# Kernel tuning notes

Measured on AMD Instinct MI355X. Metric: run time of the kernel, lower is better.

The kernel has to match this reference:

```python
import jax, jax.numpy as jnp
import numpy as np

EMBED_DIM = 1024
NUM_HEADS = 16
HEAD_DIM = EMBED_DIM // NUM_HEADS
B, L = 32, 2049
LN_EPS = 1e-5


def setup_inputs() -> dict:
    key = jax.random.key(0)
    ks = jax.random.split(key, 11)
    s = 1.0 / np.sqrt(EMBED_DIM)
    x = jax.random.normal(ks[0], (B, L, EMBED_DIM), dtype=jnp.float32)
    Wq = jax.random.normal(ks[1], (EMBED_DIM, EMBED_DIM), dtype=jnp.float32) * s
    bq = jnp.zeros((EMBED_DIM,), dtype=jnp.float32)
    Wk = jax.random.normal(ks[2], (EMBED_DIM, EMBED_DIM), dtype=jnp.float32) * s
    bk = jnp.zeros((EMBED_DIM,), dtype=jnp.float32)
    Wv = jax.random.normal(ks[3], (EMBED_DIM, EMBED_DIM), dtype=jnp.float32) * s
    bv = jnp.zeros((EMBED_DIM,), dtype=jnp.float32)
    Wo = jax.random.normal(ks[4], (EMBED_DIM, EMBED_DIM), dtype=jnp.float32) * s
    bo = jnp.zeros((EMBED_DIM,), dtype=jnp.float32)
    ln_g = jnp.ones((EMBED_DIM,), dtype=jnp.float32)
    ln_b = jnp.zeros((EMBED_DIM,), dtype=jnp.float32)
    return {"x": x, "Wq": Wq, "bq": bq, "Wk": Wk, "bk": bk, "Wv": Wv,
            "bv": bv, "Wo": Wo, "bo": bo, "ln_g": ln_g, "ln_b": ln_b}


def reference(x, Wq, bq, Wk, bk, Wv, bv, Wo, bo, ln_g, ln_b):
    # x: [B, L, D]; CLS token attends to the other L-1 tokens (dropout = eval/identity)
    cls_tok = x[:, 0, :]              # [B, D]
    others = x[:, 1:, :]              # [B, L-1, D]
    q = cls_tok @ Wq.T + bq           # [B, D]
    k = others @ Wk.T + bk            # [B, L-1, D]
    v = others @ Wv.T + bv            # [B, L-1, D]
    q = q.reshape(q.shape[0], NUM_HEADS, HEAD_DIM)                       # [B, H, d]
    k = k.reshape(k.shape[0], k.shape[1], NUM_HEADS, HEAD_DIM)           # [B, S, H, d]
    v = v.reshape(v.shape[0], v.shape[1], NUM_HEADS, HEAD_DIM)           # [B, S, H, d]
    scores = jnp.einsum('bhd,bshd->bhs', q, k) / np.sqrt(HEAD_DIM)       # [B, H, S]
    w = jax.nn.softmax(scores, axis=-1)
    attn = jnp.einsum('bhs,bshd->bhd', w, v)                             # [B, H, d]
    attn = attn.reshape(attn.shape[0], NUM_HEADS * HEAD_DIM)             # [B, D]
    out = attn @ Wo.T + bo
    y = out + cls_tok
    mu = jnp.mean(y, axis=-1, keepdims=True)
    var = jnp.var(y, axis=-1, keepdims=True)
    return (y - mu) / jnp.sqrt(var + LN_EPS) * ln_g + ln_b               # [B, D]
```

## Files before the change

kernel.cpp:

```cpp
#include <hip/hip_runtime.h>
#include <math.h>

#define B_ 32
#define L_ 2049
#define E_ 1024
#define H_ 16
#define NT_ 8
#define STILE 256

#define OFF_Q     0
#define OFF_T     (OFF_Q + B_*E_)
#define OFF_QBK   (OFF_T + B_*H_*E_)
#define OFF_M     (OFF_QBK + B_*H_)
#define OFF_L     (OFF_M + B_*NT_*H_)
#define OFF_U     (OFF_L + B_*NT_*H_)
#define OFF_ATTN  (OFF_U + B_*H_*E_)
#define OFF_Y     (OFF_ATTN + B_*E_)
#define OFF_UP    (OFF_Y + B_*E_)

__global__ __launch_bounds__(256) void k_gemm32(const float* __restrict__ A, long long As, int mode,
                                                const float* __restrict__ W,
                                                const float* __restrict__ bias,
                                                const float* __restrict__ resid, long long Rs,
                                                float* __restrict__ C) {
    __shared__ float wls[2 * 1056];
    const int j0 = blockIdx.x * 2, tid = threadIdx.x;
    #pragma unroll
    for (int k = 0; k < 2; ++k) {
        int idx4 = k * 256 + tid;
        int row = idx4 >> 8, c4 = idx4 & 255;
        float4 v = *(const float4*)(W + (size_t)(j0 + row) * E_ + 4 * c4);
        *(float4*)&wls[row * 1056 + 4 * c4 + ((c4 >> 5) << 2)] = v;
    }
    __syncthreads();
    const int bb = tid >> 3, kseg = tid & 7;
    const long long kbase = (mode == 1) ? (long long)(j0 >> 6) * E_ : 0;
    const float* arow = A + (size_t)bb * As + kbase + kseg * 128;
    float a0 = 0.f, a1 = 0.f;
    #pragma unroll 4
    for (int i = 0; i < 32; ++i) {
        float4 av = *(const float4*)(arow + 4 * i);
        const float* wb = &wls[kseg * 132 + 4 * i];
        float4 w0 = *(const float4*)(wb);
        float4 w1 = *(const float4*)(wb + 1056);
        a0 += av.x * w0.x + av.y * w0.y + av.z * w0.z + av.w * w0.w;
        a1 += av.x * w1.x + av.y * w1.y + av.z * w1.z + av.w * w1.w;
    }
    #pragma unroll
    for (int off = 4; off; off >>= 1) {
        a0 += __shfl_down(a0, off, 8);
        a1 += __shfl_down(a1, off, 8);
    }
    if (kseg == 0) {
        float r0 = a0 + bias[j0], r1 = a1 + bias[j0 + 1];
        if (resid) {
            r0 += resid[(size_t)bb * Rs + j0];
            r1 += resid[(size_t)bb * Rs + j0 + 1];
        }
        C[(size_t)bb * E_ + j0] = r0;
        C[(size_t)bb * E_ + j0 + 1] = r1;
    }
}

__global__ __launch_bounds__(256) void k_tproj(const float* __restrict__ Wk,
                                               const float* __restrict__ bk,
                                               float* __restrict__ ws) {
    __shared__ float qs[64 * 33];
    __shared__ float wls[64 * 68];
    const int h = blockIdx.x, e0 = blockIdx.y * 64, tid = threadIdx.x;
    const float* q = ws + OFF_Q;
    #pragma unroll
    for (int k = 0; k < 8; ++k) {
        int idx = k * 256 + tid;
        int b = idx >> 6, d = idx & 63;
        qs[d * 33 + b] = q[(size_t)b * E_ + 64 * h + d];
    }
    #pragma unroll
    for (int k = 0; k < 4; ++k) {
        int idx4 = k * 256 + tid;
        int d = idx4 >> 4, c4 = idx4 & 15;
        float4 v = *(const float4*)(Wk + (size_t)(64 * h + d) * E_ + e0 + 4 * c4);
        *(float4*)&wls[d * 68 + 4 * c4] = v;
    }
    __syncthreads();
    const int el = tid & 63, bq8 = tid >> 6;
    float acc[8];
    #pragma unroll
    for (int i = 0; i < 8; ++i) acc[i] = 0.f;
    for (int d = 0; d < 64; ++d) {
        float wv = wls[d * 68 + el];
        #pragma unroll
        for (int i = 0; i < 8; ++i) acc[i] += qs[d * 33 + (bq8 * 8 + i)] * wv;
    }
    float* t = ws + OFF_T;
    #pragma unroll
    for (int i = 0; i < 8; ++i)
        t[((size_t)(bq8 * 8 + i) * H_ + h) * E_ + e0 + el] = acc[i] * 0.125f;
    if (e0 == 0 && tid < 32) {
        float s = 0.f;
        for (int d = 0; d < 64; ++d) s += qs[d * 33 + tid] * bk[64 * h + d];
        ws[OFF_QBK + tid * H_ + h] = s * 0.125f;
    }
}

__global__ __launch_bounds__(1024) void k_attn_core(const float* __restrict__ x,
                                                    float* __restrict__ ws) {
    const int tile = blockIdx.x, b = blockIdx.y, tid = threadIdx.x;
    const int s0t = tile * STILE;
    const float* tmat = ws + OFF_T + (size_t)b * H_ * E_;
    const float* xb = x + (size_t)(b * L_ + 1 + s0t) * E_;

    __shared__ float smem[16384];
    __shared__ float wl[256 * 16];
    __shared__ float pmax[128], psum[128], msh[16];

    const int lane = tid & 63, w = tid >> 6;
    const int g = lane & 3, ssub = lane >> 2;
    const int wlo = w & 7;
    const int ehalf = (w >> 3) * 512;
    const int sA = 32 * wlo + ssub, sB = sA + 16;

    #pragma unroll
    for (int k = 0; k < 4; ++k) {
        int idx4 = k * 1024 + tid;
        *(float4*)&smem[4 * idx4] = *(const float4*)(tmat + 4 * idx4);
    }
    __syncthreads();

    float acc[16][2];
    #pragma unroll
    for (int h = 0; h < 16; ++h) { acc[h][0] = 0.f; acc[h][1] = 0.f; }

    {
        const float* xA = xb + (size_t)sA * E_ + ehalf + 4 * g;
        const float* xB = xb + (size_t)sB * E_ + ehalf + 4 * g;
        const float* tb = &smem[ehalf + 4 * g];
        #pragma unroll 2
        for (int c = 0; c < 32; ++c) {
            float4 a0 = *(const float4*)(xA + 16 * c);
            float4 b0 = *(const float4*)(xB + 16 * c);
            #pragma unroll
            for (int h = 0; h < 16; ++h) {
                float4 t0 = *(const float4*)(tb + h * E_ + 16 * c);
                acc[h][0] += t0.x * a0.x + t0.y * a0.y + t0.z * a0.z + t0.w * a0.w;
                acc[h][1] += t0.x * b0.x + t0.y * b0.y + t0.z * b0.z + t0.w * b0.w;
            }
        }
    }
    #pragma unroll
    for (int h = 0; h < 16; ++h) {
        #pragma unroll
        for (int s = 0; s < 2; ++s) {
            float v = acc[h][s];
            v += __shfl_xor(v, 1, 64);
            v += __shfl_xor(v, 2, 64);
            acc[h][s] = v;
        }
    }
    if (w >= 8) {
        if (g == 0) {
            *(float4*)&wl[sA * 16 + 0]  = make_float4(acc[0][0], acc[1][0], acc[2][0], acc[3][0]);
            *(float4*)&wl[sB * 16 + 0]  = make_float4(acc[0][1], acc[1][1], acc[2][1], acc[3][1]);
        } else if (g == 1) {
            *(float4*)&wl[sA * 16 + 4]  = make_float4(acc[4][0], acc[5][0], acc[6][0], acc[7][0]);
            *(float4*)&wl[sB * 16 + 4]  = make_float4(acc[4][1], acc[5][1], acc[6][1], acc[7][1]);
        } else if (g == 2) {
            *(float4*)&wl[sA * 16 + 8]  = make_float4(acc[8][0], acc[9][0], acc[10][0], acc[11][0]);
            *(float4*)&wl[sB * 16 + 8]  = make_float4(acc[8][1], acc[9][1], acc[10][1], acc[11][1]);
        } else {
            *(float4*)&wl[sA * 16 + 12] = make_float4(acc[12][0], acc[13][0], acc[14][0], acc[15][0]);
            *(float4*)&wl[sB * 16 + 12] = make_float4(acc[12][1], acc[13][1], acc[14][1], acc[15][1]);
        }
    }
    __syncthreads();

    if (w < 8) {
        const float* qbkp = ws + OFF_QBK + b * H_;
        #pragma unroll
        for (int h = 0; h < 16; ++h) {
            float qb = qbkp[h];
            acc[h][0] += wl[sA * 16 + h] + qb;
            acc[h][1] += wl[sB * 16 + h] + qb;
        }
        #pragma unroll
        for (int h = 0; h < 16; ++h) {
            float v = fmaxf(acc[h][0], acc[h][1]);
            v = fmaxf(v, __shfl_xor(v, 4, 64));
            v = fmaxf(v, __shfl_xor(v, 8, 64));
            v = fmaxf(v, __shfl_xor(v, 16, 64));
            v = fmaxf(v, __shfl_xor(v, 32, 64));
            if (lane == 0) pmax[w * 16 + h] = v;
        }
    }
    __syncthreads();
    if (tid < 16) {
        float M = pmax[tid];
        #pragma unroll
        for (int q = 1; q < 8; ++q) M = fmaxf(M, pmax[q * 16 + tid]);
        msh[tid] = M;
        ws[OFF_M + (size_t)(b * NT_ + tile) * H_ + tid] = M;
    }
    __syncthreads();
    if (w < 8) {
        float ex0[16], ex1[16];
        #pragma unroll
        for (int h = 0; h < 16; ++h) {
            float M = msh[h];
            ex0[h] = __expf(acc[h][0] - M);
            ex1[h] = __expf(acc[h][1] - M);
        }
        if (g == 0) {
            *(float4*)&wl[sA * 16 + 0]  = make_float4(ex0[0], ex0[1], ex0[2], ex0[3]);
            *(float4*)&wl[sB * 16 + 0]  = make_float4(ex1[0], ex1[1], ex1[2], ex1[3]);
        } else if (g == 1) {
            *(float4*)&wl[sA * 16 + 4]  = make_float4(ex0[4], ex0[5], ex0[6], ex0[7]);
            *(float4*)&wl[sB * 16 + 4]  = make_float4(ex1[4], ex1[5], ex1[6], ex1[7]);
        } else if (g == 2) {
            *(float4*)&wl[sA * 16 + 8]  = make_float4(ex0[8], ex0[9], ex0[10], ex0[11]);
            *(float4*)&wl[sB * 16 + 8]  = make_float4(ex1[8], ex1[9], ex1[10], ex1[11]);
        } else {
            *(float4*)&wl[sA * 16 + 12] = make_float4(ex0[12], ex0[13], ex0[14], ex0[15]);
            *(float4*)&wl[sB * 16 + 12] = make_float4(ex1[12], ex1[13], ex1[14], ex1[15]);
        }
        #pragma unroll
        for (int h = 0; h < 16; ++h) {
            float v = ex0[h] + ex1[h];
            v += __shfl_xor(v, 4, 64);
            v += __shfl_xor(v, 8, 64);
            v += __shfl_xor(v, 16, 64);
            v += __shfl_xor(v, 32, 64);
            if (lane == 0) psum[w * 16 + h] = v;
        }
    }
    __syncthreads();
    if (tid < 16) {
        float Ls = 0.f;
        #pragma unroll
        for (int q = 0; q < 8; ++q) Ls += psum[q * 16 + tid];
        ws[OFF_L + (size_t)(b * NT_ + tile) * H_ + tid] = Ls;
    }

    const int hp = w & 7, shalf = w >> 3;
    float4 accA[4], accB[4];
    #pragma unroll
    for (int j = 0; j < 4; ++j) {
        accA[j] = make_float4(0.f, 0.f, 0.f, 0.f);
        accB[j] = make_float4(0.f, 0.f, 0.f, 0.f);
    }
    const int r0 = tid >> 8, c4 = tid & 255;
    float4 st0 = *(const float4*)(xb + (size_t)(r0)     * E_ + 4 * c4);
    float4 st1 = *(const float4*)(xb + (size_t)(r0 + 4) * E_ + 4 * c4);
    *(float4*)&smem[(r0)     * 1024 + 4 * c4] = st0;
    *(float4*)&smem[(r0 + 4) * 1024 + 4 * c4] = st1;
    for (int c = 0; c < 32; ++c) {
        __syncthreads();
        if (c + 1 < 32) {
            st0 = *(const float4*)(xb + (size_t)(8 * (c + 1) + r0)     * E_ + 4 * c4);
            st1 = *(const float4*)(xb + (size_t)(8 * (c + 1) + r0 + 4) * E_ + 4 * c4);
        }
        const float* A = &smem[(c & 1) * 8192];
        #pragma unroll
        for (int rr = 0; rr < 4; ++rr) {
            const int r = 4 * shalf + rr;
            float2 wv = *(const float2*)&wl[(8 * c + r) * 16 + 2 * hp];
            #pragma unroll
            for (int ej = 0; ej < 4; ++ej) {
                float4 xv = *(const float4*)&A[r * 1024 + 4 * lane + 256 * ej];
                accA[ej].x += wv.x * xv.x; accA[ej].y += wv.x * xv.y;
                accA[ej].z += wv.x * xv.z; accA[ej].w += wv.x * xv.w;
                accB[ej].x += wv.y * xv.x; accB[ej].y += wv.y * xv.y;
                accB[ej].z += wv.y * xv.z; accB[ej].w += wv.y * xv.w;
            }
        }
        if (c + 1 < 32) {
            float* D = &smem[((c + 1) & 1) * 8192];
            *(float4*)&D[(r0)     * 1024 + 4 * c4] = st0;
            *(float4*)&D[(r0 + 4) * 1024 + 4 * c4] = st1;
        }
    }
    __syncthreads();
    if (shalf == 1) {
        #pragma unroll
        for (int ej = 0; ej < 4; ++ej) {
            *(float4*)&smem[hp * 2048 +        4 * lane + 256 * ej] = accA[ej];
            *(float4*)&smem[hp * 2048 + 1024 + 4 * lane + 256 * ej] = accB[ej];
        }
    }
    __syncthreads();
    if (shalf == 0) {
        float* up = ws + OFF_UP + ((size_t)(b * NT_ + tile) * H_ + 2 * hp) * E_;
        #pragma unroll
        for (int ej = 0; ej < 4; ++ej) {
            float4 pA = *(const float4*)&smem[hp * 2048 +        4 * lane + 256 * ej];
            float4 pB = *(const float4*)&smem[hp * 2048 + 1024 + 4 * lane + 256 * ej];
            float4 oA = make_float4(accA[ej].x + pA.x, accA[ej].y + pA.y,
                                    accA[ej].z + pA.z, accA[ej].w + pA.w);
            float4 oB = make_float4(accB[ej].x + pB.x, accB[ej].y + pB.y,
                                    accB[ej].z + pB.z, accB[ej].w + pB.w);
            *(float4*)(up +       4 * lane + 256 * ej) = oA;
            *(float4*)(up + E_ +  4 * lane + 256 * ej) = oB;
        }
    }
}

__global__ __launch_bounds__(256) void k_combine(float* __restrict__ ws) {
    const int b = blockIdx.x, h = blockIdx.y, tid = threadIdx.x;
    float m[NT_], l[NT_], f[NT_];
    float M = -1e30f;
    #pragma unroll
    for (int tg = 0; tg < NT_; ++tg) {
        m[tg] = ws[OFF_M + (b * NT_ + tg) * H_ + h];
        l[tg] = ws[OFF_L + (b * NT_ + tg) * H_ + h];
        M = fmaxf(M, m[tg]);
    }
    float Ls = 0.f;
    #pragma unroll
    for (int tg = 0; tg < NT_; ++tg) {
        f[tg] = __expf(m[tg] - M);
        Ls += f[tg] * l[tg];
    }
    const float inv = 1.f / Ls;
    float4 a = make_float4(0.f, 0.f, 0.f, 0.f);
    #pragma unroll
    for (int tg = 0; tg < NT_; ++tg) {
        float4 v = *(const float4*)(ws + OFF_UP + (size_t)((b * NT_ + tg) * H_ + h) * E_ + 4 * tid);
        a.x += f[tg] * v.x; a.y += f[tg] * v.y; a.z += f[tg] * v.z; a.w += f[tg] * v.w;
    }
    a.x *= inv; a.y *= inv; a.z *= inv; a.w *= inv;
    *(float4*)(ws + OFF_U + (size_t)(b * H_ + h) * E_ + 4 * tid) = a;
}

__global__ __launch_bounds__(256) void k_ln(const float* __restrict__ ws,
                                            const float* __restrict__ g,
                                            const float* __restrict__ be,
                                            float* __restrict__ out) {
    const int b = blockIdx.x, tid = threadIdx.x;
    const float* y = ws + OFF_Y + (size_t)b * E_;
    float4 v = *(const float4*)(y + 4 * tid);
    float s = v.x + v.y + v.z + v.w;
    float s2 = v.x * v.x + v.y * v.y + v.z * v.z + v.w * v.w;
    for (int o = 32; o; o >>= 1) {
        s += __shfl_down(s, o, 64);
        s2 += __shfl_down(s2, o, 64);
    }
    __shared__ float rs[4], rs2[4];
    int ww = tid >> 6;
    if ((tid & 63) == 0) { rs[ww] = s; rs2[ww] = s2; }
    __syncthreads();
    float S = rs[0] + rs[1] + rs[2] + rs[3];
    float S2 = rs2[0] + rs2[1] + rs2[2] + rs2[3];
    float mean = S * (1.f / 1024.f);
    float var = S2 * (1.f / 1024.f) - mean * mean;
    float r = rsqrtf(var + 1e-5f);
    float4 gv = *(const float4*)(g + 4 * tid);
    float4 bb2 = *(const float4*)(be + 4 * tid);
    float4 o;
    o.x = (v.x - mean) * r * gv.x + bb2.x;
    o.y = (v.y - mean) * r * gv.y + bb2.y;
    o.z = (v.z - mean) * r * gv.z + bb2.z;
    o.w = (v.w - mean) * r * gv.w + bb2.w;
    *(float4*)(out + (size_t)b * E_ + 4 * tid) = o;
}

extern "C" void kernel_launch(void* const* d_in, const int* in_sizes, int n_in,
                              void* d_out, int out_size, void* d_ws, size_t ws_size,
                              hipStream_t stream) {
    const float* x  = (const float*)d_in[0];
    const float* Wq = (const float*)d_in[1];
    const float* bq = (const float*)d_in[2];
    const float* Wk = (const float*)d_in[3];
    const float* bk = (const float*)d_in[4];
    const float* Wv = (const float*)d_in[5];
    const float* bv = (const float*)d_in[6];
    const float* Wo = (const float*)d_in[7];
    const float* bo = (const float*)d_in[8];
    const float* g  = (const float*)d_in[9];
    const float* be = (const float*)d_in[10];
    float* ws = (float*)d_ws;
    float* out = (float*)d_out;

    k_gemm32<<<512, 256, 0, stream>>>(x, (long long)L_ * E_, 0, Wq, bq, nullptr, 0, ws + OFF_Q);
    k_tproj<<<dim3(16, 16), 256, 0, stream>>>(Wk, bk, ws);
    k_attn_core<<<dim3(NT_, B_), 1024, 0, stream>>>(x, ws);
    k_combine<<<dim3(B_, H_), 256, 0, stream>>>(ws);
    k_gemm32<<<512, 256, 0, stream>>>(ws + OFF_U, (long long)H_ * E_, 1, Wv, bv, nullptr, 0, ws + OFF_ATTN);
    k_gemm32<<<512, 256, 0, stream>>>(ws + OFF_ATTN, (long long)E_, 0, Wo, bo, x, (long long)L_ * E_, ws + OFF_Y);
    k_ln<<<B_, 256, 0, stream>>>(ws, g, be, out);
}
```

Measured before the change: 489.1 us.

## Retile attention-core score and PV loops for higher register reuse per load

The score phase now gives each wave 8 heads by 4 sequence rows instead of 16 heads by 2 rows, so each shared-memory T load is reused across four x rows. The PV phase has each wave compute 8 heads over a 256-wide column slice, so one x float4 load feeds eight head accumulators instead of two. The aim is fewer LDS and global loads per FMA in both phases. It changes the partial-reduction layout, adds unroll 1 on the score loop, and may shift register pressure.

```diff
diff --git a/kernel.cpp b/kernel.cpp
--- a/kernel.cpp
+++ b/kernel.cpp
@@ -112,13 +112,10 @@
 
     __shared__ float smem[16384];
     __shared__ float wl[256 * 16];
-    __shared__ float pmax[128], psum[128], msh[16];
+    __shared__ float pmax[64], psum[64], msh[16];
 
     const int lane = tid & 63, w = tid >> 6;
     const int g = lane & 3, ssub = lane >> 2;
-    const int wlo = w & 7;
-    const int ehalf = (w >> 3) * 512;
-    const int sA = 32 * wlo + ssub, sB = sA + 16;
 
     #pragma unroll
     for (int k = 0; k < 4; ++k) {
@@ -127,126 +124,128 @@
     }
     __syncthreads();
 
-    float acc[16][2];
-    #pragma unroll
-    for (int h = 0; h < 16; ++h) { acc[h][0] = 0.f; acc[h][1] = 0.f; }
+    const int eh1 = w >> 3, hh1 = (w >> 2) & 1, sq1 = w & 3;
+    const int hbase1 = hh1 * 8;
+    const int srow0 = sq1 * 64 + 4 * ssub;
+
+    float acc[8][4];
+    #pragma unroll
+    for (int h = 0; h < 8; ++h) { acc[h][0] = 0.f; acc[h][1] = 0.f; acc[h][2] = 0.f; acc[h][3] = 0.f; }
 
     {
-        const float* xA = xb + (size_t)sA * E_ + ehalf + 4 * g;
-        const float* xB = xb + (size_t)sB * E_ + ehalf + 4 * g;
-        const float* tb = &smem[ehalf + 4 * g];
-        #pragma unroll 2
+        const float* xq = xb + (size_t)srow0 * E_ + eh1 * 512 + 4 * g;
+        const float* tb = &smem[hbase1 * E_ + eh1 * 512 + 4 * g];
+        #pragma unroll 1
         for (int c = 0; c < 32; ++c) {
-            float4 a0 = *(const float4*)(xA + 16 * c);
-            float4 b0 = *(const float4*)(xB + 16 * c);
+            const int e0 = 16 * c;
+            float4 x0 = *(const float4*)(xq + e0);
+            float4 x1 = *(const float4*)(xq + E_ + e0);
+            float4 x2 = *(const float4*)(xq + 2 * E_ + e0);
+            float4 x3 = *(const float4*)(xq + 3 * E_ + e0);
             #pragma unroll
-            for (int h = 0; h < 16; ++h) {
-                float4 t0 = *(const float4*)(tb + h * E_ + 16 * c);
-                acc[h][0] += t0.x * a0.x + t0.y * a0.y + t0.z * a0.z + t0.w * a0.w;
-                acc[h][1] += t0.x * b0.x + t0.y * b0.y + t0.z * b0.z + t0.w * b0.w;
+            for (int h = 0; h < 8; ++h) {
+                float4 t0 = *(const float4*)(tb + h * E_ + e0);
+                acc[h][0] += t0.x * x0.x + t0.y * x0.y + t0.z * x0.z + t0.w * x0.w;
+                acc[h][1] += t0.x * x1.x + t0.y * x1.y + t0.z * x1.z + t0.w * x1.w;
+                acc[h][2] += t0.x * x2.x + t0.y * x2.y + t0.z * x2.z + t0.w * x2.w;
+                acc[h][3] += t0.x * x3.x + t0.y * x3.y + t0.z * x3.z + t0.w * x3.w;
             }
         }
     }
     #pragma unroll
-    for (int h = 0; h < 16; ++h) {
-        #pragma unroll
-        for (int s = 0; s < 2; ++s) {
-            float v = acc[h][s];
+    for (int h = 0; h < 8; ++h) {
+        #pragma unroll
+        for (int k = 0; k < 4; ++k) {
+            float v = acc[h][k];
             v += __shfl_xor(v, 1, 64);
             v += __shfl_xor(v, 2, 64);
-            acc[h][s] = v;
-        }
-    }
-    if (w >= 8) {
-        if (g == 0) {
-            *(float4*)&wl[sA * 16 + 0]  = make_float4(acc[0][0], acc[1][0], acc[2][0], acc[3][0]);
-            *(float4*)&wl[sB * 16 + 0]  = make_float4(acc[0][1], acc[1][1], acc[2][1], acc[3][1]);
-        } else if (g == 1) {
-            *(float4*)&wl[sA * 16 + 4]  = make_float4(acc[4][0], acc[5][0], acc[6][0], acc[7][0]);
-            *(float4*)&wl[sB * 16 + 4]  = make_float4(acc[4][1], acc[5][1], acc[6][1], acc[7][1]);
-        } else if (g == 2) {
-            *(float4*)&wl[sA * 16 + 8]  = make_float4(acc[8][0], acc[9][0], acc[10][0], acc[11][0]);
-            *(float4*)&wl[sB * 16 + 8]  = make_float4(acc[8][1], acc[9][1], acc[10][1], acc[11][1]);
-        } else {
-            *(float4*)&wl[sA * 16 + 12] = make_float4(acc[12][0], acc[13][0], acc[14][0], acc[15][0]);
-            *(float4*)&wl[sB * 16 + 12] = make_float4(acc[12][1], acc[13][1], acc[14][1], acc[15][1]);
-        }
-    }
-    __syncthreads();
-
-    if (w < 8) {
+            acc[h][k] = v;
+        }
+    }
+    if (eh1 == 1) {
+        #pragma unroll
+        for (int k = 0; k < 4; ++k) {
+            float2* dst = (float2*)&wl[(srow0 + k) * 16 + hbase1];
+            if (g == 0)      dst[0] = make_float2(acc[0][k], acc[1][k]);
+            else if (g == 1) dst[1] = make_float2(acc[2][k], acc[3][k]);
+            else if (g == 2) dst[2] = make_float2(acc[4][k], acc[5][k]);
+            else             dst[3] = make_float2(acc[6][k], acc[7][k]);
+        }
+    }
+    __syncthreads();
+
+    if (eh1 == 0) {
         const float* qbkp = ws + OFF_QBK + b * H_;
         #pragma unroll
-        for (int h = 0; h < 16; ++h) {
-            float qb = qbkp[h];
-            acc[h][0] += wl[sA * 16 + h] + qb;
-            acc[h][1] += wl[sB * 16 + h] + qb;
-        }
-        #pragma unroll
-        for (int h = 0; h < 16; ++h) {
-            float v = fmaxf(acc[h][0], acc[h][1]);
+        for (int k = 0; k < 4; ++k) {
+            const float* src = &wl[(srow0 + k) * 16 + hbase1];
+            float4 p0 = *(const float4*)(src);
+            float4 p1 = *(const float4*)(src + 4);
+            acc[0][k] += p0.x; acc[1][k] += p0.y; acc[2][k] += p0.z; acc[3][k] += p0.w;
+            acc[4][k] += p1.x; acc[5][k] += p1.y; acc[6][k] += p1.z; acc[7][k] += p1.w;
+        }
+        #pragma unroll
+        for (int h = 0; h < 8; ++h) {
+            float qb = qbkp[hbase1 + h];
+            acc[h][0] += qb; acc[h][1] += qb; acc[h][2] += qb; acc[h][3] += qb;
+            float v = fmaxf(fmaxf(acc[h][0], acc[h][1]), fmaxf(acc[h][2], acc[h][3]));
             v = fmaxf(v, __shfl_xor(v, 4, 64));
             v = fmaxf(v, __shfl_xor(v, 8, 64));
             v = fmaxf(v, __shfl_xor(v, 16, 64));
             v = fmaxf(v, __shfl_xor(v, 32, 64));
-            if (lane == 0) pmax[w * 16 + h] = v;
+            if (lane == 0) pmax[sq1 * 16 + hbase1 + h] = v;
         }
     }
     __syncthreads();
     if (tid < 16) {
         float M = pmax[tid];
-        #pragma unroll
-        for (int q = 1; q < 8; ++q) M = fmaxf(M, pmax[q * 16 + tid]);
+        M = fmaxf(M, pmax[16 + tid]);
+        M = fmaxf(M, pmax[32 + tid]);
+        M = fmaxf(M, pmax[48 + tid]);
         msh[tid] = M;
         ws[OFF_M + (size_t)(b * NT_ + tile) * H_ + tid] = M;
     }
     __syncthreads();
-    if (w < 8) {
-        float ex0[16], ex1[16];
-        #pragma unroll
-        for (int h = 0; h < 16; ++h) {
-            float M = msh[h];
-            ex0[h] = __expf(acc[h][0] - M);
-            ex1[h] = __expf(acc[h][1] - M);
-        }
-        if (g == 0) {
-            *(float4*)&wl[sA * 16 + 0]  = make_float4(ex0[0], ex0[1], ex0[2], ex0[3]);
-            *(float4*)&wl[sB * 16 + 0]  = make_float4(ex1[0], ex1[1], ex1[2], ex1[3]);
-        } else if (g == 1) {
-            *(float4*)&wl[sA * 16 + 4]  = make_float4(ex0[4], ex0[5], ex0[6], ex0[7]);
-            *(float4*)&wl[sB * 16 + 4]  = make_float4(ex1[4], ex1[5], ex1[6], ex1[7]);
-        } else if (g == 2) {
-            *(float4*)&wl[sA * 16 + 8]  = make_float4(ex0[8], ex0[9], ex0[10], ex0[11]);
-            *(float4*)&wl[sB * 16 + 8]  = make_float4(ex1[8], ex1[9], ex1[10], ex1[11]);
-        } else {
-            *(float4*)&wl[sA * 16 + 12] = make_float4(ex0[12], ex0[13], ex0[14], ex0[15]);
-            *(float4*)&wl[sB * 16 + 12] = make_float4(ex1[12], ex1[13], ex1[14], ex1[15]);
-        }
-        #pragma unroll
-        for (int h = 0; h < 16; ++h) {
-            float v = ex0[h] + ex1[h];
+    if (eh1 == 0) {
+        #pragma unroll
+        for (int h = 0; h < 8; ++h) {
+            float M = msh[hbase1 + h];
+            acc[h][0] = __expf(acc[h][0] - M);
+            acc[h][1] = __expf(acc[h][1] - M);
+            acc[h][2] = __expf(acc[h][2] - M);
+            acc[h][3] = __expf(acc[h][3] - M);
+        }
+        #pragma unroll
+        for (int k = 0; k < 4; ++k) {
+            float2* dst = (float2*)&wl[(srow0 + k) * 16 + hbase1];
+            if (g == 0)      dst[0] = make_float2(acc[0][k], acc[1][k]);
+            else if (g == 1) dst[1] = make_float2(acc[2][k], acc[3][k]);
+            else if (g == 2) dst[2] = make_float2(acc[4][k], acc[5][k]);
+            else             dst[3] = make_float2(acc[6][k], acc[7][k]);
+        }
+        #pragma unroll
+        for (int h = 0; h < 8; ++h) {
+            float v = acc[h][0] + acc[h][1] + acc[h][2] + acc[h][3];
             v += __shfl_xor(v, 4, 64);
             v += __shfl_xor(v, 8, 64);
             v += __shfl_xor(v, 16, 64);
             v += __shfl_xor(v, 32, 64);
-            if (lane == 0) psum[w * 16 + h] = v;
+            if (lane == 0) psum[sq1 * 16 + hbase1 + h] = v;
         }
     }
     __syncthreads();
     if (tid < 16) {
-        float Ls = 0.f;
-        #pragma unroll
-        for (int q = 0; q < 8; ++q) Ls += psum[q * 16 + tid];
+        float Ls = psum[tid] + psum[16 + tid] + psum[32 + tid] + psum[48 + tid];
         ws[OFF_L + (size_t)(b * NT_ + tile) * H_ + tid] = Ls;
     }
 
-    const int hp = w & 7, shalf = w >> 3;
-    float4 accA[4], accB[4];
-    #pragma unroll
-    for (int j = 0; j < 4; ++j) {
-        accA[j] = make_float4(0.f, 0.f, 0.f, 0.f);
-        accB[j] = make_float4(0.f, 0.f, 0.f, 0.f);
-    }
+    const int hb2 = (w >> 3) * 8;
+    const int sh2 = (w >> 2) & 1;
+    const int eqb = (w & 3) * 256;
+    float4 acc2[8];
+    #pragma unroll
+    for (int j = 0; j < 8; ++j) acc2[j] = make_float4(0.f, 0.f, 0.f, 0.f);
+
     const int r0 = tid >> 8, c4 = tid & 255;
     float4 st0 = *(const float4*)(xb + (size_t)(r0)     * E_ + 4 * c4);
     float4 st1 = *(const float4*)(xb + (size_t)(r0 + 4) * E_ + 4 * c4);
@@ -261,16 +260,19 @@
         const float* A = &smem[(c & 1) * 8192];
         #pragma unroll
         for (int rr = 0; rr < 4; ++rr) {
-            const int r = 4 * shalf + rr;
-            float2 wv = *(const float2*)&wl[(8 * c + r) * 16 + 2 * hp];
-            #pragma unroll
-            for (int ej = 0; ej < 4; ++ej) {
-                float4 xv = *(const float4*)&A[r * 1024 + 4 * lane + 256 * ej];
-                accA[ej].x += wv.x * xv.x; accA[ej].y += wv.x * xv.y;
-                accA[ej].z += wv.x * xv.z; accA[ej].w += wv.x * xv.w;
-                accB[ej].x += wv.y * xv.x; accB[ej].y += wv.y * xv.y;
-                accB[ej].z += wv.y * xv.z; accB[ej].w += wv.y * xv.w;
-            }
+            const int r = 4 * sh2 + rr;
+            const float* wrow = &wl[(8 * c + r) * 16 + hb2];
+            float4 w0 = *(const float4*)(wrow);
+            float4 w1 = *(const float4*)(wrow + 4);
+            float4 xv = *(const float4*)&A[r * 1024 + eqb + 4 * lane];
+            acc2[0].x += w0.x * xv.x; acc2[0].y += w0.x * xv.y; acc2[0].z += w0.x * xv.z; acc2[0].w += w0.x * xv.w;
+            acc2[1].x += w0.y * xv.x; acc2[1].y += w0.y * xv.y; acc2[1].z += w0.y * xv.z; acc2[1].w += w0.y * xv.w;
+            acc2[2].x += w0.z * xv.x; acc2[2].y += w0.z * xv.y; acc2[2].z += w0.z * xv.z; acc2[2].w += w0.z * xv.w;
+            acc2[3].x += w0.w * xv.x; acc2[3].y += w0.w * xv.y; acc2[3].z += w0.w * xv.z; acc2[3].w += w0.w * xv.w;
+            acc2[4].x += w1.x * xv.x; acc2[4].y += w1.x * xv.y; acc2[4].z += w1.x * xv.z; acc2[4].w += w1.x * xv.w;
+            acc2[5].x += w1.y * xv.x; acc2[5].y += w1.y * xv.y; acc2[5].z += w1.y * xv.z; acc2[5].w += w1.y * xv.w;
+            acc2[6].x += w1.z * xv.x; acc2[6].y += w1.z * xv.y; acc2[6].z += w1.z * xv.z; acc2[6].w += w1.z * xv.w;
+            acc2[7].x += w1.w * xv.x; acc2[7].y += w1.w * xv.y; acc2[7].z += w1.w * xv.z; acc2[7].w += w1.w * xv.w;
         }
         if (c + 1 < 32) {
             float* D = &smem[((c + 1) & 1) * 8192];
@@ -279,26 +281,22 @@
         }
     }
     __syncthreads();
-    if (shalf == 1) {
-        #pragma unroll
-        for (int ej = 0; ej < 4; ++ej) {
-            *(float4*)&smem[hp * 2048 +        4 * lane + 256 * ej] = accA[ej];
-            *(float4*)&smem[hp * 2048 + 1024 + 4 * lane + 256 * ej] = accB[ej];
-        }
-    }
-    __syncthreads();
-    if (shalf == 0) {
-        float* up = ws + OFF_UP + ((size_t)(b * NT_ + tile) * H_ + 2 * hp) * E_;
-        #pragma unroll
-        for (int ej = 0; ej < 4; ++ej) {
-            float4 pA = *(const float4*)&smem[hp * 2048 +        4 * lane + 256 * ej];
-            float4 pB = *(const float4*)&smem[hp * 2048 + 1024 + 4 * lane + 256 * ej];
-            float4 oA = make_float4(accA[ej].x + pA.x, accA[ej].y + pA.y,
-                                    accA[ej].z + pA.z, accA[ej].w + pA.w);
-            float4 oB = make_float4(accB[ej].x + pB.x, accB[ej].y + pB.y,
-                                    accB[ej].z + pB.z, accB[ej].w + pB.w);
-            *(float4*)(up +       4 * lane + 256 * ej) = oA;
-            *(float4*)(up + E_ +  4 * lane + 256 * ej) = oB;
+    if (sh2 == 1) {
+        float* pl = &smem[((w >> 3) * 4 + (w & 3)) * 2048];
+        #pragma unroll
+        for (int h = 0; h < 8; ++h)
+            *(float4*)&pl[h * 256 + 4 * lane] = acc2[h];
+    }
+    __syncthreads();
+    if (sh2 == 0) {
+        const float* pl = &smem[((w >> 3) * 4 + (w & 3)) * 2048];
+        float* up = ws + OFF_UP + ((size_t)(b * NT_ + tile) * H_ + hb2) * E_ + eqb;
+        #pragma unroll
+        for (int h = 0; h < 8; ++h) {
+            float4 pv = *(const float4*)&pl[h * 256 + 4 * lane];
+            float4 o = make_float4(acc2[h].x + pv.x, acc2[h].y + pv.y,
+                                   acc2[h].z + pv.z, acc2[h].w + pv.w);
+            *(float4*)(up + (size_t)h * E_ + 4 * lane) = o;
         }
     }
 }
```

Result: no change. 490.5 us (+0.3%).

## Compute per-tile weighted x sums directly from global memory per column

Applied to the files above, without the earlier changes.

Replaces the LDS double-buffered staging of x rows and the two-half split reduction with a per-thread column loop. Each thread owns one embedding column, reads x values straight from global memory (register-prefetched by 8 rows), and accumulates all 16 head weights read from LDS. This removes the shared-memory x staging, the per-chunk barriers and the final cross-half reduction. In exchange it relies on scalar coalesced global loads and uses more accumulator registers per thread.

```diff
diff --git a/kernel.cpp b/kernel.cpp
--- a/kernel.cpp
+++ b/kernel.cpp
@@ -240,67 +240,43 @@
         ws[OFF_L + (size_t)(b * NT_ + tile) * H_ + tid] = Ls;
     }
 
-    const int hp = w & 7, shalf = w >> 3;
-    float4 accA[4], accB[4];
-    #pragma unroll
-    for (int j = 0; j < 4; ++j) {
-        accA[j] = make_float4(0.f, 0.f, 0.f, 0.f);
-        accB[j] = make_float4(0.f, 0.f, 0.f, 0.f);
-    }
-    const int r0 = tid >> 8, c4 = tid & 255;
-    float4 st0 = *(const float4*)(xb + (size_t)(r0)     * E_ + 4 * c4);
-    float4 st1 = *(const float4*)(xb + (size_t)(r0 + 4) * E_ + 4 * c4);
-    *(float4*)&smem[(r0)     * 1024 + 4 * c4] = st0;
-    *(float4*)&smem[(r0 + 4) * 1024 + 4 * c4] = st1;
-    for (int c = 0; c < 32; ++c) {
-        __syncthreads();
-        if (c + 1 < 32) {
-            st0 = *(const float4*)(xb + (size_t)(8 * (c + 1) + r0)     * E_ + 4 * c4);
-            st1 = *(const float4*)(xb + (size_t)(8 * (c + 1) + r0 + 4) * E_ + 4 * c4);
-        }
-        const float* A = &smem[(c & 1) * 8192];
-        #pragma unroll
-        for (int rr = 0; rr < 4; ++rr) {
-            const int r = 4 * shalf + rr;
-            float2 wv = *(const float2*)&wl[(8 * c + r) * 16 + 2 * hp];
+    float uacc[16];
+    #pragma unroll
+    for (int h = 0; h < 16; ++h) uacc[h] = 0.f;
+
+    const float* xcol = xb + 64 * w + lane;
+    float xv[8], xn[8];
+    #pragma unroll
+    for (int k = 0; k < 8; ++k) xv[k] = xcol[(size_t)k * E_];
+    for (int rb = 0; rb < 32; ++rb) {
+        const int rbase = rb * 8;
+        if (rb + 1 < 32) {
             #pragma unroll
-            for (int ej = 0; ej < 4; ++ej) {
-                float4 xv = *(const float4*)&A[r * 1024 + 4 * lane + 256 * ej];
-                accA[ej].x += wv.x * xv.x; accA[ej].y += wv.x * xv.y;
-                accA[ej].z += wv.x * xv.z; accA[ej].w += wv.x * xv.w;
-                accB[ej].x += wv.y * xv.x; accB[ej].y += wv.y * xv.y;
-                accB[ej].z += wv.y * xv.z; accB[ej].w += wv.y * xv.w;
-            }
-        }
-        if (c + 1 < 32) {
-            float* D = &smem[((c + 1) & 1) * 8192];
-            *(float4*)&D[(r0)     * 1024 + 4 * c4] = st0;
-            *(float4*)&D[(r0 + 4) * 1024 + 4 * c4] = st1;
-        }
-    }
-    __syncthreads();
-    if (shalf == 1) {
-        #pragma unroll
-        for (int ej = 0; ej < 4; ++ej) {
-            *(float4*)&smem[hp * 2048 +        4 * lane + 256 * ej] = accA[ej];
-            *(float4*)&smem[hp * 2048 + 1024 + 4 * lane + 256 * ej] = accB[ej];
-        }
-    }
-    __syncthreads();
-    if (shalf == 0) {
-        float* up = ws + OFF_UP + ((size_t)(b * NT_ + tile) * H_ + 2 * hp) * E_;
-        #pragma unroll
-        for (int ej = 0; ej < 4; ++ej) {
-            float4 pA = *(const float4*)&smem[hp * 2048 +        4 * lane + 256 * ej];
-            float4 pB = *(const float4*)&smem[hp * 2048 + 1024 + 4 * lane + 256 * ej];
-            float4 oA = make_float4(accA[ej].x + pA.x, accA[ej].y + pA.y,
-                                    accA[ej].z + pA.z, accA[ej].w + pA.w);
-            float4 oB = make_float4(accB[ej].x + pB.x, accB[ej].y + pB.y,
-                                    accB[ej].z + pB.z, accB[ej].w + pB.w);
-            *(float4*)(up +       4 * lane + 256 * ej) = oA;
-            *(float4*)(up + E_ +  4 * lane + 256 * ej) = oB;
-        }
-    }
+            for (int k = 0; k < 8; ++k) xn[k] = xcol[(size_t)(rbase + 8 + k) * E_];
+        }
+        #pragma unroll
+        for (int k = 0; k < 8; ++k) {
+            const float* wrow = &wl[(rbase + k) * 16];
+            float4 w0 = *(const float4*)(wrow);
+            float4 w1 = *(const float4*)(wrow + 4);
+            float4 w2 = *(const float4*)(wrow + 8);
+            float4 w3 = *(const float4*)(wrow + 12);
+            const float xs = xv[k];
+            uacc[0]  += w0.x * xs; uacc[1]  += w0.y * xs;
+            uacc[2]  += w0.z * xs; uacc[3]  += w0.w * xs;
+            uacc[4]  += w1.x * xs; uacc[5]  += w1.y * xs;
+            uacc[6]  += w1.z * xs; uacc[7]  += w1.w * xs;
+            uacc[8]  += w2.x * xs; uacc[9]  += w2.y * xs;
+            uacc[10] += w2.z * xs; uacc[11] += w2.w * xs;
+            uacc[12] += w3.x * xs; uacc[13] += w3.y * xs;
+            uacc[14] += w3.z * xs; uacc[15] += w3.w * xs;
+        }
+        #pragma unroll
+        for (int k = 0; k < 8; ++k) xv[k] = xn[k];
+    }
+    float* up = ws + OFF_UP + ((size_t)((b * NT_ + tile) * H_)) * E_ + 64 * w + lane;
+    #pragma unroll
+    for (int h = 0; h < 16; ++h) up[(size_t)h * E_] = uacc[h];
 }
 
 __global__ __launch_bounds__(256) void k_combine(float* __restrict__ ws) {
```

Result: no change. 490.2 us (+0.2%).
